# Performance work log

Measured on AMD Instinct MI355X. Metric: run time of the kernel, lower is better.

The kernel has to match this reference:

```python
import jax, jax.numpy as jnp
import numpy as np

B, C, DD, HH, WW = 1, 128, 16, 16, 16
D_STATE, D_CONV, EXPAND = 16, 4, 2
D_INNER = EXPAND * C
DT_RANK = (C + 15) // 16


def setup_inputs():
    key = jax.random.key(0)
    ks = jax.random.split(key, 10)
    def w(k, shape, s=0.02):
        return jax.random.normal(k, shape, dtype=jnp.float32) * s
    return {
        "x": jax.random.normal(ks[0], (B, C, DD, HH, WW), dtype=jnp.float32),
        "ln_w": jnp.ones((C,), jnp.float32),
        "ln_b": jnp.zeros((C,), jnp.float32),
        "mnorm_w": jnp.ones((C,), jnp.float32),
        "mnorm_b": jnp.zeros((C,), jnp.float32),
        "in_proj_w": w(ks[1], (2 * D_INNER, C)),
        "conv_w": w(ks[2], (D_INNER, D_CONV), 0.2),
        "conv_b": jnp.zeros((D_INNER,), jnp.float32),
        "x_proj_w": w(ks[3], (DT_RANK + 2 * D_STATE, D_INNER)),
        "dt_proj_w": w(ks[4], (D_INNER, DT_RANK), 0.1),
        "dt_proj_b": jnp.full((D_INNER,), float(np.log(np.expm1(0.01))), jnp.float32),
        "A_log": jnp.log(jnp.tile(jnp.arange(1, D_STATE + 1, dtype=jnp.float32), (D_INNER, 1))),
        "D_param": jnp.ones((D_INNER,), jnp.float32),
        "out_proj_w": w(ks[5], (C, D_INNER)),
        "proj_w": w(ks[6], (C, 3 * C)),
        "proj_b": jnp.zeros((C,), jnp.float32),
        "fc1_w": w(ks[7], (4 * C, C)),
        "fc1_b": jnp.zeros((4 * C,), jnp.float32),
        "fc2_w": w(ks[8], (C, 4 * C)),
        "fc2_b": jnp.zeros((C,), jnp.float32),
    }


def _ln_cf(x, w, b, eps=1e-6):
    # channels_first LayerNorm over axis 1 (matches custom LayerNorm)
    u = x.mean(1, keepdims=True)
    s = ((x - u) ** 2).mean(1, keepdims=True)
    xn = (x - u) * jax.lax.rsqrt(s + eps)
    return w[None, :, None, None, None] * xn + b[None, :, None, None, None]


def _ln_last(x, w, b, eps=1e-5):
    u = x.mean(-1, keepdims=True)
    s = ((x - u) ** 2).mean(-1, keepdims=True)
    return (x - u) * jax.lax.rsqrt(s + eps) * w + b


def _selective_scan(u, delta, A, Bm, Cm, Dv):
    # u, delta: (N,L,d); Bm,Cm: (N,L,n); A: (d,n); Dv: (d,)
    dA = jnp.exp(delta[..., None] * A)                               # (N,L,d,n)
    dBu = delta[..., None] * Bm[:, :, None, :] * u[..., None]         # (N,L,d,n)
    def step(h, inp):
        dA_t, dBu_t, C_t = inp
        h = dA_t * h + dBu_t
        y = jnp.einsum("bdn,bn->bd", h, C_t)
        return h, y
    h0 = jnp.zeros((u.shape[0], A.shape[0], A.shape[1]), u.dtype)
    _, ys = jax.lax.scan(step, h0, (dA.swapaxes(0, 1), dBu.swapaxes(0, 1), Cm.swapaxes(0, 1)))
    return ys.swapaxes(0, 1) + u * Dv


def _mamba(xin, in_proj_w, conv_w, conv_b, x_proj_w, dt_proj_w, dt_proj_b, A_log, D_param, out_proj_w):
    # xin: (N, L, C)
    N, L, _ = xin.shape
    xz = xin @ in_proj_w.T                                            # (N,L,2*d_inner)
    xr, z = jnp.split(xz, 2, axis=-1)
    # causal depthwise conv1d, kernel D_CONV, left-padded (mamba conv1d[..., :L])
    xp = jnp.pad(xr, ((0, 0), (D_CONV - 1, 0), (0, 0)))
    xc = sum(conv_w[:, k] * xp[:, k:k + L, :] for k in range(D_CONV)) + conv_b
    xc = jax.nn.silu(xc)
    x_dbl = xc @ x_proj_w.T                                           # (N,L,dt_rank+2n)
    dt = x_dbl[..., :DT_RANK]
    Bm = x_dbl[..., DT_RANK:DT_RANK + D_STATE]
    Cm = x_dbl[..., DT_RANK + D_STATE:]
    delta = jax.nn.softplus(dt @ dt_proj_w.T + dt_proj_b)
    A = -jnp.exp(A_log)
    y = _selective_scan(xc, delta, A, Bm, Cm, D_param)
    y = y * jax.nn.silu(z)
    return y @ out_proj_w.T


def _forward(x, ln_w, ln_b, mnorm_w, mnorm_b, in_proj_w, conv_w, conv_b, x_proj_w, dt_proj_w, dt_proj_b, A_log, D_param, out_proj_w, proj_w, proj_b, fc1_w, fc1_b, fc2_w, fc2_b):
    Bb, Cc, Dd, Hh, Ww = x.shape
    L = Dd * Hh * Ww
    x1 = _ln_cf(x, ln_w, ln_b)
    # three directional flattenings (d-, h-, w-major); cube => shapes identical
    xd = x1.reshape(Bb, Cc, L)
    xh = x1.transpose(0, 1, 3, 4, 2).reshape(Bb, Cc, L)
    xw = x1.transpose(0, 1, 4, 2, 3).reshape(Bb, Cc, L)
    seq = jnp.stack([xd, xh, xw], 0).reshape(3 * Bb, Cc, L).swapaxes(1, 2)  # (3B,L,C)
    seq = _ln_last(seq, mnorm_w, mnorm_b)
    y = _mamba(seq, in_proj_w, conv_w, conv_b, x_proj_w, dt_proj_w, dt_proj_b, A_log, D_param, out_proj_w)
    # reassemble per-direction volumes (no inverse permute, matching torch code) and concat on channels
    cat = y.swapaxes(1, 2).reshape(3, Bb, Cc, Dd, Hh, Ww).transpose(1, 0, 2, 3, 4, 5).reshape(Bb, 3 * Cc, Dd, Hh, Ww)
    out1 = jnp.einsum("bkdhw,ok->bodhw", cat, proj_w) + proj_b[None, :, None, None, None]
    out_res = x + out1
    h = _ln_cf(out_res, ln_w, ln_b)
    h = jnp.einsum("bcdhw,oc->bodhw", h, fc1_w) + fc1_b[None, :, None, None, None]
    h = jax.nn.gelu(h, approximate=False)
    h = jnp.einsum("bcdhw,oc->bodhw", h, fc2_w) + fc2_b[None, :, None, None, None]
    return h + out_res


def reference(x, ln_w, ln_b, mnorm_w, mnorm_b, in_proj_w, conv_w, conv_b, x_proj_w, dt_proj_w, dt_proj_b, A_log, D_param, out_proj_w, proj_w, proj_b, fc1_w, fc1_b, fc2_w, fc2_b):
    return _forward(x, ln_w, ln_b, mnorm_w, mnorm_b, in_proj_w, conv_w, conv_b, x_proj_w, dt_proj_w, dt_proj_b, A_log, D_param, out_proj_w, proj_w, proj_b, fc1_w, fc1_b, fc2_w, fc2_b)
```

## Files before the change

### kernel.cpp

```cpp
#include <hip/hip_runtime.h>
#include <hip/hip_bf16.h>
#include <math.h>

#define L 4096
#define C 128
#define DI 256
#define NST 16
#define NS 3
#define NCH 256
#define CT 16
#define R3 12288

__device__ __forceinline__ float siluf(float x){ return x / (1.f + __expf(-x)); }
__device__ __forceinline__ float geluf(float x){ return 0.5f*x*(1.f + erff(x*0.70710678118654752f)); }

__device__ __forceinline__ int permf(int s, int l){
  if(s==0) return l;
  if(s==1) return ((l&15)<<8) | ((l>>8)<<4) | ((l>>4)&15);
  return (((l>>4)&15)<<8) | ((l&15)<<4) | (l>>8);
}

__global__ void k_M(const float* __restrict__ opw, const float* __restrict__ pw,
                    float* __restrict__ Mw){
  int b = blockIdx.x;
  int o = b & 127, s = b >> 7;
  int d = threadIdx.x;
  float acc = 0.f;
  for(int c=0;c<C;c++) acc += opw[c*DI + d] * pw[o*384 + s*128 + c];
  Mw[(s*256+d)*128 + o] = acc;
}

__global__ void k_lngemm(const float* __restrict__ x, const float* __restrict__ lw,
                         const float* __restrict__ lb, const float* __restrict__ mw,
                         const float* __restrict__ mb, const float* __restrict__ ipw,
                         float* __restrict__ Z){
  __shared__ float As[128][68];
  __shared__ float Bs[64][132];
  int p0 = blockIdx.x*64, j0 = blockIdx.y*64;
  int tid = threadIdx.x;
  for(int q=0;q<8;q++){
    int f = q*1024 + tid*4; int cc = f>>6, p = f&63;
    float4 v = *(const float4*)&x[cc*L + p0 + p];
    *(float4*)&As[cc][p] = v;
  }
  for(int q=0;q<8;q++){
    int f = q*1024 + tid*4; int j = f>>7, k = f&127;
    float4 b = *(const float4*)&ipw[(j0+j)*C + k];
    *(float4*)&Bs[j][k] = b;
  }
  __syncthreads();
  {
    int p = tid>>2, kg = tid&3;
    float s=0.f, sq=0.f;
    #pragma unroll
    for(int i=0;i<32;i++){
      int k = kg*32 + ((i + kg*2)&31);
      float v = As[k][p]; s += v; sq += v*v;
    }
    s  += __shfl_xor(s,1);  s  += __shfl_xor(s,2);
    sq += __shfl_xor(sq,1); sq += __shfl_xor(sq,2);
    float m1 = s*(1.f/C);
    float r1 = rsqrtf(sq*(1.f/C) - m1*m1 + 1e-6f);
    float s2=0.f, sq2=0.f;
    #pragma unroll
    for(int i=0;i<32;i++){
      int k = kg*32 + ((i + kg*2)&31);
      float t = lw[k]*((As[k][p]-m1)*r1) + lb[k];
      s2 += t; sq2 += t*t;
    }
    s2  += __shfl_xor(s2,1);  s2  += __shfl_xor(s2,2);
    sq2 += __shfl_xor(sq2,1); sq2 += __shfl_xor(sq2,2);
    float m2 = s2*(1.f/C);
    float r2 = rsqrtf(sq2*(1.f/C) - m2*m2 + 1e-5f);
    #pragma unroll
    for(int i=0;i<32;i++){
      int k = kg*32 + ((i + kg*2)&31);
      float t = lw[k]*((As[k][p]-m1)*r1) + lb[k];
      As[k][p] = mw[k]*((t-m2)*r2) + mb[k];
    }
  }
  __syncthreads();
  int og = tid & 15, r4 = tid >> 4;
  float acc[4][4] = {};
  for(int k=0;k<128;k++){
    float4 av = *(const float4*)&As[k][r4*4];
    float a[4] = {av.x, av.y, av.z, av.w};
    float b[4];
    #pragma unroll
    for(int j=0;j<4;j++) b[j] = Bs[og+16*j][k];
    #pragma unroll
    for(int i=0;i<4;i++)
      #pragma unroll
      for(int j=0;j<4;j++) acc[i][j] += a[i]*b[j];
  }
  #pragma unroll
  for(int i=0;i<4;i++)
    #pragma unroll
    for(int j=0;j<4;j++)
      Z[(p0+r4*4+i)*512 + j0 + og + 16*j] = acc[i][j];
}

__global__ void k_conv(const float* __restrict__ Z, const float* __restrict__ cw,
                       const float* __restrict__ cb, float* __restrict__ xc){
  int bl = blockIdx.x;
  int s = bl >> 12, l = bl & 4095;
  int d = threadIdx.x;
  float acc = cb[d];
  #pragma unroll
  for(int k=0;k<4;k++){
    int lk = l - 3 + k;
    if(lk >= 0){
      int p = permf(s, lk);
      acc += cw[d*4+k] * Z[p*512 + d];
    }
  }
  xc[bl*DI + d] = siluf(acc);
}

__global__ void k_xd3(const float* __restrict__ xc, const float* __restrict__ xpw,
                      const float* __restrict__ dtw, const float* __restrict__ dtb,
                      float* __restrict__ Bc, float* __restrict__ Cc,
                      float* __restrict__ delta){
  __shared__ float Ast[256][65];
  __shared__ float BCs[40][65];
  int r0 = blockIdx.x*64;
  int tid = threadIdx.x;
  for(int q=0;q<16;q++){
    int f = q*1024 + tid*4; int row = f>>8, k = f&255;
    float4 v = *(const float4*)&xc[(r0+row)*DI + k];
    Ast[k+0][row]=v.x; Ast[k+1][row]=v.y; Ast[k+2][row]=v.z; Ast[k+3][row]=v.w;
  }
  __syncthreads();
  int lane = tid & 63;
  int cb0 = __builtin_amdgcn_readfirstlane((tid>>6)*10);
  const float* wp = xpw + cb0*DI;
  float acc[10] = {0.f,0.f,0.f,0.f,0.f,0.f,0.f,0.f,0.f,0.f};
  for(int k4=0;k4<64;k4++){
    int k = k4*4;
    float a0 = Ast[k+0][lane], a1 = Ast[k+1][lane];
    float a2 = Ast[k+2][lane], a3 = Ast[k+3][lane];
    #pragma unroll
    for(int j=0;j<10;j++){
      float4 w = *(const float4*)&wp[j*DI + k];
      acc[j] += a0*w.x + a1*w.y + a2*w.z + a3*w.w;
    }
  }
  #pragma unroll
  for(int j=0;j<10;j++) BCs[cb0+j][lane] = acc[j];
  __syncthreads();
  {
    float4 ww0 = *(const float4*)&dtw[tid*8];
    float4 ww1 = *(const float4*)&dtw[tid*8+4];
    float bb = dtb[tid];
    for(int r=0;r<64;r++){
      float aa = bb + BCs[0][r]*ww0.x + BCs[1][r]*ww0.y + BCs[2][r]*ww0.z + BCs[3][r]*ww0.w
                    + BCs[4][r]*ww1.x + BCs[5][r]*ww1.y + BCs[6][r]*ww1.z + BCs[7][r]*ww1.w;
      delta[(r0+r)*DI + tid] = (aa > 20.f) ? aa : log1pf(__expf(aa));
    }
  }
  {
    int r = tid>>2, ng = (tid&3)*4;
    float4 bv = make_float4(BCs[ 8+ng][r], BCs[ 9+ng][r], BCs[10+ng][r], BCs[11+ng][r]);
    float4 cv = make_float4(BCs[24+ng][r], BCs[25+ng][r], BCs[26+ng][r], BCs[27+ng][r]);
    *(float4*)&Bc[(r0+r)*NST + ng] = bv;
    *(float4*)&Cc[(r0+r)*NST + ng] = cv;
  }
}

__global__ void k_scanA(const float* __restrict__ delta, const float* __restrict__ xc,
                        const float* __restrict__ Bc, const float* __restrict__ A_log,
                        float* __restrict__ aggA, float* __restrict__ aggB){
  int b = blockIdx.x;
  int ng = b & 3, ch = (b>>2)&255, s = b>>10;
  int d = threadIdx.x;
  int n0 = ng*4;
  float Aa[4], P[4] = {1.f,1.f,1.f,1.f}, S[4] = {0.f,0.f,0.f,0.f};
  #pragma unroll
  for(int j=0;j<4;j++) Aa[j] = -__expf(A_log[d*NST + n0 + j]);
  int base = s*L + ch*CT;
  #pragma unroll
  for(int st=0; st<CT; st++){
    int row = base + st;
    float dl = delta[row*DI + d];
    float u  = xc[row*DI + d];
    float4 bv = *(const float4*)&Bc[row*NST + n0];
    float dlu = dl*u;
    float a;
    a = __expf(dl*Aa[0]); S[0] = a*S[0] + dlu*bv.x; P[0] *= a;
    a = __expf(dl*Aa[1]); S[1] = a*S[1] + dlu*bv.y; P[1] *= a;
    a = __expf(dl*Aa[2]); S[2] = a*S[2] + dlu*bv.z; P[2] *= a;
    a = __expf(dl*Aa[3]); S[3] = a*S[3] + dlu*bv.w; P[3] *= a;
  }
  int idx0 = ch*R3 + s*256 + d;
  #pragma unroll
  for(int j=0;j<4;j++){
    int idx = idx0 + (n0+j)*768;
    aggA[idx] = P[j]; aggB[idx] = S[j];
  }
}

__global__ void k_scanB(const float* __restrict__ aggA, const float* __restrict__ aggB,
                        float* __restrict__ hIn){
  __shared__ float PA[32][9], PB[32][9];
  int tid = threadIdx.x;
  int jl = tid & 31, seg = tid >> 5;
  int j = blockIdx.x*32 + jl;
  int c0 = seg*32;
  float pa[32], pb[32];
  float P = 1.f, S = 0.f;
  #pragma unroll
  for(int i=0;i<32;i++){
    pa[i] = P; pb[i] = S;
    float a = aggA[(c0+i)*R3 + j], b = aggB[(c0+i)*R3 + j];
    S = a*S + b; P = a*P;
  }
  PA[jl][seg] = P; PB[jl][seg] = S;
  __syncthreads();
  if(tid < 32){
    float h = 0.f;
    #pragma unroll
    for(int sg=0; sg<8; sg++){
      float p = PA[tid][sg], s2 = PB[tid][sg];
      PA[tid][sg] = h;
      h = p*h + s2;
    }
  }
  __syncthreads();
  float h0 = PA[jl][seg];
  #pragma unroll
  for(int i=0;i<32;i++){
    hIn[(c0+i)*R3 + j] = pa[i]*h0 + pb[i];
  }
}

__global__ void k_scanC(const float* __restrict__ delta, const float* __restrict__ xc,
                        const float* __restrict__ Bc, const float* __restrict__ Cc,
                        const float* __restrict__ A_log, const float* __restrict__ Dp,
                        const float* __restrict__ Z, const float* __restrict__ hIn,
                        float* __restrict__ yz){
  int b = blockIdx.x;
  int ch = b & 255, s = b >> 8;
  int d = threadIdx.x;
  float Aa[16], h[16];
  #pragma unroll
  for(int n=0;n<16;n++) Aa[n] = -__expf(A_log[d*NST + n]);
  #pragma unroll
  for(int n=0;n<16;n++) h[n] = hIn[ch*R3 + n*768 + s*256 + d];
  float Dv = Dp[d];
  int base = s*L + ch*CT;
  #pragma unroll 2
  for(int st=0; st<CT; st++){
    int row = base + st;
    float dl = delta[row*DI + d];
    float u  = xc[row*DI + d];
    float dlu = dl*u;
    const float4* Bp = (const float4*)&Bc[row*NST];
    const float4* Cp = (const float4*)&Cc[row*NST];
    float y = u*Dv;
    #pragma unroll
    for(int q=0;q<4;q++){
      float4 bv = Bp[q], cv = Cp[q];
      float a;
      a = __expf(dl*Aa[4*q+0]); h[4*q+0] = a*h[4*q+0] + dlu*bv.x; y += h[4*q+0]*cv.x;
      a = __expf(dl*Aa[4*q+1]); h[4*q+1] = a*h[4*q+1] + dlu*bv.y; y += h[4*q+1]*cv.y;
      a = __expf(dl*Aa[4*q+2]); h[4*q+2] = a*h[4*q+2] + dlu*bv.z; y += h[4*q+2]*cv.z;
      a = __expf(dl*Aa[4*q+3]); h[4*q+3] = a*h[4*q+3] + dlu*bv.w; y += h[4*q+3]*cv.w;
    }
    int l = ch*CT + st;
    int p = permf(s, l);
    float zv = Z[p*512 + 256 + d];
    yz[(s*L + l)*DI + d] = y * siluf(zv);
  }
}

__global__ void k_proj(const float* __restrict__ yz, const float* __restrict__ Mw,
                       float* __restrict__ pp){
  __shared__ float As[64][68];
  __shared__ float Bs[64][132];
  int p0 = blockIdx.x*64; int kc = blockIdx.y;
  int s = kc >> 1, d0 = (kc & 1)*128;
  int tid = threadIdx.x;
  int og = tid & 15, r4 = tid >> 4;
  float acc[4][8] = {};
  for(int kk=0; kk<2; kk++){
    int kb = d0 + kk*64;
    for(int q=0;q<4;q++){
      int f = q*1024 + tid*4; int r = f>>6, k = f&63;
      float4 a = *(const float4*)&yz[(s*L + p0 + r)*DI + kb + k];
      *(float4*)&As[r][k] = a;
    }
    for(int q=0;q<8;q++){
      int f = q*1024 + tid*4; int k = f>>7, o = f&127;
      float4 b = *(const float4*)&Mw[(s*256 + kb + k)*128 + o];
      *(float4*)&Bs[k][o] = b;
    }
    __syncthreads();
    for(int k=0;k<64;k++){
      float a[4];
      #pragma unroll
      for(int i=0;i<4;i++) a[i] = As[r4*4+i][k];
      #pragma unroll
      for(int j=0;j<8;j++){
        float bb = Bs[k][og+16*j];
        #pragma unroll
        for(int i=0;i<4;i++) acc[i][j] += a[i]*bb;
      }
    }
    __syncthreads();
  }
  float* dst = pp + kc*524288;
  #pragma unroll
  for(int i=0;i<4;i++)
    #pragma unroll
    for(int j=0;j<8;j++)
      dst[(p0+r4*4+i)*C + og + 16*j] = acc[i][j];
}

__global__ void k_pred(const float* __restrict__ pp, const float* __restrict__ x,
                       const float* __restrict__ pb, float* __restrict__ ores){
  __shared__ float Xs[16][129];
  int p0 = blockIdx.x*16; int tid = threadIdx.x;
  for(int q=0;q<8;q++){
    int f = q*256 + tid; int pl = f&15, o = f>>4;
    Xs[pl][o] = x[o*L + p0 + pl];
  }
  __syncthreads();
  for(int q=0;q<8;q++){
    int f = q*256 + tid; int o = f&127, pl = f>>7;
    int idx = (p0+pl)*C + o;
    float v = pp[idx] + pp[524288+idx] + pp[1048576+idx]
            + pp[1572864+idx] + pp[2097152+idx] + pp[2621440+idx];
    ores[idx] = v + Xs[pl][o] + pb[o];
  }
}

__global__ void k_fc1(const float* __restrict__ ores, const float* __restrict__ lw,
                      const float* __restrict__ lb, const float* __restrict__ w1,
                      const float* __restrict__ b1, float* __restrict__ H){
  __shared__ float As[64][129];
  __shared__ float Bs[64][129];
  int p0 = blockIdx.x*64, j0 = blockIdx.y*64;
  int tid = threadIdx.x;
  for(int q=0;q<8;q++){
    int f = q*1024 + tid*4; int r = f>>7, k = f&127;
    float4 a = *(const float4*)&ores[(p0+r)*C + k];
    As[r][k]=a.x; As[r][k+1]=a.y; As[r][k+2]=a.z; As[r][k+3]=a.w;
    float4 b = *(const float4*)&w1[(j0+r)*C + k];
    Bs[r][k]=b.x; Bs[r][k+1]=b.y; Bs[r][k+2]=b.z; Bs[r][k+3]=b.w;
  }
  __syncthreads();
  {
    int r = tid>>2, kg = tid&3;
    float s=0.f, sq=0.f;
    #pragma unroll
    for(int i=0;i<32;i++){
      int k = kg*32 + ((i + kg*8)&31);
      float v = As[r][k]; s += v; sq += v*v;
    }
    s  += __shfl_xor(s,1);  s  += __shfl_xor(s,2);
    sq += __shfl_xor(sq,1); sq += __shfl_xor(sq,2);
    float m1 = s*(1.f/C);
    float r1 = rsqrtf(sq*(1.f/C) - m1*m1 + 1e-6f);
    #pragma unroll
    for(int i=0;i<32;i++){
      int k = kg*32 + ((i + kg*8)&31);
      As[r][k] = lw[k]*((As[r][k]-m1)*r1) + lb[k];
    }
  }
  __syncthreads();
  int og = tid & 15, r4 = tid >> 4;
  float acc[4][4] = {};
  for(int k=0;k<128;k++){
    float a[4], b[4];
    #pragma unroll
    for(int i=0;i<4;i++) a[i] = As[r4*4+i][k];
    #pragma unroll
    for(int j=0;j<4;j++) b[j] = Bs[og+16*j][k];
    #pragma unroll
    for(int i=0;i<4;i++)
      #pragma unroll
      for(int j=0;j<4;j++) acc[i][j] += a[i]*b[j];
  }
  #pragma unroll
  for(int i=0;i<4;i++)
    #pragma unroll
    for(int j=0;j<4;j++){
      int jj = j0 + og + 16*j;
      H[(p0+r4*4+i)*512 + jj] = geluf(acc[i][j] + b1[jj]);
    }
}

__global__ void k_fc2(const float* __restrict__ H, const float* __restrict__ w2,
                      float* __restrict__ fp){
  __shared__ float As[64][68];
  __shared__ float Bs[128][68];
  int p0 = blockIdx.x*64; int kc = blockIdx.y;
  int tid = threadIdx.x;
  int og = tid & 15, r4 = tid >> 4;
  float acc[4][8] = {};
  for(int kk=0; kk<2; kk++){
    int kb = kc*128 + kk*64;
    for(int q=0;q<4;q++){
      int f = q*1024 + tid*4; int r = f>>6, k = f&63;
      float4 a = *(const float4*)&H[(p0+r)*512 + kb + k];
      *(float4*)&As[r][k] = a;
    }
    for(int q=0;q<8;q++){
      int f = q*1024 + tid*4; int o = f>>6, k = f&63;
      float4 b = *(const float4*)&w2[o*512 + kb + k];
      *(float4*)&Bs[o][k] = b;
    }
    __syncthreads();
    for(int k=0;k<64;k++){
      float a[4];
      #pragma unroll
      for(int i=0;i<4;i++) a[i] = As[r4*4+i][k];
      #pragma unroll
      for(int j=0;j<8;j++){
        float bb = Bs[og+16*j][k];
        #pragma unroll
        for(int i=0;i<4;i++) acc[i][j] += a[i]*bb;
      }
    }
    __syncthreads();
  }
  float* dst = fp + kc*524288;
  #pragma unroll
  for(int i=0;i<4;i++)
    #pragma unroll
    for(int j=0;j<8;j++)
      dst[(p0+r4*4+i)*C + og + 16*j] = acc[i][j];
}

__global__ void k_fred(const float* __restrict__ fp, const float* __restrict__ b2,
                       const float* __restrict__ ores, float* __restrict__ out){
  __shared__ float S[128][17];
  int p0 = blockIdx.x*16; int tid = threadIdx.x;
  for(int q=0;q<8;q++){
    int f = q*256 + tid; int o = f&127, pl = f>>7;
    int idx = (p0+pl)*C + o;
    float v = fp[idx] + fp[524288+idx] + fp[1048576+idx] + fp[1572864+idx];
    S[o][pl] = v + b2[o] + ores[idx];
  }
  __syncthreads();
  for(int q=0;q<8;q++){
    int f = q*256 + tid; int pl = f&15, o = f>>4;
    out[o*L + p0 + pl] = S[o][pl];
  }
}

extern "C" void kernel_launch(void* const* d_in, const int* in_sizes, int n_in,
                              void* d_out, int out_size, void* d_ws, size_t ws_size,
                              hipStream_t stream) {
  const float* x     = (const float*)d_in[0];
  const float* ln_w  = (const float*)d_in[1];
  const float* ln_b  = (const float*)d_in[2];
  const float* mw    = (const float*)d_in[3];
  const float* mb    = (const float*)d_in[4];
  const float* ipw   = (const float*)d_in[5];
  const float* cw    = (const float*)d_in[6];
  const float* cb    = (const float*)d_in[7];
  const float* xpw   = (const float*)d_in[8];
  const float* dtw   = (const float*)d_in[9];
  const float* dtb   = (const float*)d_in[10];
  const float* A_log = (const float*)d_in[11];
  const float* Dp    = (const float*)d_in[12];
  const float* opw   = (const float*)d_in[13];
  const float* pw    = (const float*)d_in[14];
  const float* pb    = (const float*)d_in[15];
  const float* w1    = (const float*)d_in[16];
  const float* b1    = (const float*)d_in[17];
  const float* w2    = (const float*)d_in[18];
  const float* b2    = (const float*)d_in[19];
  float* out = (float*)d_out;

  float* ws = (float*)d_ws;
  float* Z     = ws;
  float* xc    = Z     + 2097152;
  float* delta = xc    + 3145728;
  float* dt    = delta + 3145728;
  float* Bc    = dt    + 98304;
  float* Cc    = Bc    + 196608;
  float* aggA  = Cc    + 196608;
  float* aggB  = aggA  + 3145728;
  float* hIn   = aggB  + 3145728;
  float* Mw    = hIn   + 3145728;
  float* ores  = Mw    + 98304;
  (void)dt;
  float* yz = aggA;
  float* pp = delta;
  float* H  = Z;
  float* fp = xc;

  k_M     <<<384, 256, 0, stream>>>(opw, pw, Mw);
  k_lngemm<<<dim3(64,8), 256, 0, stream>>>(x, ln_w, ln_b, mw, mb, ipw, Z);
  k_conv  <<<NS*L, 256, 0, stream>>>(Z, cw, cb, xc);
  k_xd3   <<<192, 256, 0, stream>>>(xc, xpw, dtw, dtb, Bc, Cc, delta);
  k_scanA <<<3072, 256, 0, stream>>>(delta, xc, Bc, A_log, aggA, aggB);
  k_scanB <<<384, 256, 0, stream>>>(aggA, aggB, hIn);
  k_scanC <<<768, 256, 0, stream>>>(delta, xc, Bc, Cc, A_log, Dp, Z, hIn, yz);
  k_proj  <<<dim3(64,6), 256, 0, stream>>>(yz, Mw, pp);
  k_pred  <<<256, 256, 0, stream>>>(pp, x, pb, ores);
  k_fc1   <<<dim3(64,8), 256, 0, stream>>>(ores, ln_w, ln_b, w1, b1, H);
  k_fc2   <<<dim3(64,4), 256, 0, stream>>>(H, w2, fp);
  k_fred  <<<256, 256, 0, stream>>>(fp, b2, ores, out);
}
```

Measured before the change: 292.6 us.

## Split x_proj GEMM into split-K tiled kernel plus separate dt/B/C epilogue

Replaces the single 192-block x_proj+dt_proj kernel with two kernels. The first computes partial x_proj products with split-K over two halves, using 768 blocks with shared-memory tiles of activations and weights. The second sums the partials and applies dt_proj, softplus and the B/C scatter over 768 blocks. This raises parallelism on a kernel that under-filled the GPU, at the cost of an extra launch and an intermediate buffer round-trip through global memory.

Result: faster. 274.3 us (-6.3%).

```diff
diff --git a/kernel.cpp b/kernel.cpp
--- a/kernel.cpp
+++ b/kernel.cpp
@@ -117,53 +117,71 @@
   xc[bl*DI + d] = siluf(acc);
 }
 
-__global__ void k_xd3(const float* __restrict__ xc, const float* __restrict__ xpw,
-                      const float* __restrict__ dtw, const float* __restrict__ dtb,
-                      float* __restrict__ Bc, float* __restrict__ Cc,
-                      float* __restrict__ delta){
-  __shared__ float Ast[256][65];
-  __shared__ float BCs[40][65];
-  int r0 = blockIdx.x*64;
-  int tid = threadIdx.x;
-  for(int q=0;q<16;q++){
-    int f = q*1024 + tid*4; int row = f>>8, k = f&255;
-    float4 v = *(const float4*)&xc[(r0+row)*DI + k];
-    Ast[k+0][row]=v.x; Ast[k+1][row]=v.y; Ast[k+2][row]=v.z; Ast[k+3][row]=v.w;
-  }
-  __syncthreads();
-  int lane = tid & 63;
-  int cb0 = __builtin_amdgcn_readfirstlane((tid>>6)*10);
-  const float* wp = xpw + cb0*DI;
-  float acc[10] = {0.f,0.f,0.f,0.f,0.f,0.f,0.f,0.f,0.f,0.f};
-  for(int k4=0;k4<64;k4++){
-    int k = k4*4;
-    float a0 = Ast[k+0][lane], a1 = Ast[k+1][lane];
-    float a2 = Ast[k+2][lane], a3 = Ast[k+3][lane];
-    #pragma unroll
-    for(int j=0;j<10;j++){
-      float4 w = *(const float4*)&wp[j*DI + k];
-      acc[j] += a0*w.x + a1*w.y + a2*w.z + a3*w.w;
-    }
-  }
-  #pragma unroll
-  for(int j=0;j<10;j++) BCs[cb0+j][lane] = acc[j];
+__global__ void k_xd4a(const float* __restrict__ xc, const float* __restrict__ xpw,
+                       float* __restrict__ xp){
+  __shared__ float As[32][132];
+  __shared__ float Ws[40][132];
+  int r0 = blockIdx.x*32;
+  int k0 = blockIdx.y*128;
+  int tid = threadIdx.x;
+  for(int q=0;q<4;q++){
+    int f = q*256 + tid; int r = f>>5, kk = (f&31)*4;
+    float4 v = *(const float4*)&xc[(r0+r)*DI + k0 + kk];
+    *(float4*)&As[r][kk] = v;
+  }
+  for(int q=0;q<5;q++){
+    int f = q*256 + tid; int col = f>>5, kk = (f&31)*4;
+    float4 v = *(const float4*)&xpw[col*DI + k0 + kk];
+    *(float4*)&Ws[col][kk] = v;
+  }
+  __syncthreads();
+  int r = tid & 31, cg = tid >> 5;
+  float acc[5] = {0.f,0.f,0.f,0.f,0.f};
+  for(int k4=0;k4<32;k4++){
+    float4 a = *(const float4*)&As[r][k4*4];
+    #pragma unroll
+    for(int j=0;j<5;j++){
+      float4 w = *(const float4*)&Ws[cg*5+j][k4*4];
+      acc[j] += a.x*w.x + a.y*w.y + a.z*w.z + a.w*w.w;
+    }
+  }
+  float* dst = xp + (blockIdx.y*12288 + r0 + r)*40 + cg*5;
+  #pragma unroll
+  for(int j=0;j<5;j++) dst[j] = acc[j];
+}
+
+__global__ void k_xd4b(const float* __restrict__ xp, const float* __restrict__ dtw,
+                       const float* __restrict__ dtb, float* __restrict__ Bc,
+                       float* __restrict__ Cc, float* __restrict__ delta){
+  __shared__ float xdb[40][17];
+  int r0 = blockIdx.x*16;
+  int tid = threadIdx.x;
+  for(int e=tid; e<640; e+=256){
+    int row = e/40, col = e%40;
+    int idx = (r0+row)*40 + col;
+    xdb[col][row] = xp[idx] + xp[491520 + idx];
+  }
   __syncthreads();
   {
     float4 ww0 = *(const float4*)&dtw[tid*8];
     float4 ww1 = *(const float4*)&dtw[tid*8+4];
     float bb = dtb[tid];
-    for(int r=0;r<64;r++){
-      float aa = bb + BCs[0][r]*ww0.x + BCs[1][r]*ww0.y + BCs[2][r]*ww0.z + BCs[3][r]*ww0.w
-                    + BCs[4][r]*ww1.x + BCs[5][r]*ww1.y + BCs[6][r]*ww1.z + BCs[7][r]*ww1.w;
+    #pragma unroll 4
+    for(int r=0;r<16;r++){
+      float aa = bb + xdb[0][r]*ww0.x + xdb[1][r]*ww0.y + xdb[2][r]*ww0.z + xdb[3][r]*ww0.w
+                    + xdb[4][r]*ww1.x + xdb[5][r]*ww1.y + xdb[6][r]*ww1.z + xdb[7][r]*ww1.w;
       delta[(r0+r)*DI + tid] = (aa > 20.f) ? aa : log1pf(__expf(aa));
     }
   }
-  {
-    int r = tid>>2, ng = (tid&3)*4;
-    float4 bv = make_float4(BCs[ 8+ng][r], BCs[ 9+ng][r], BCs[10+ng][r], BCs[11+ng][r]);
-    float4 cv = make_float4(BCs[24+ng][r], BCs[25+ng][r], BCs[26+ng][r], BCs[27+ng][r]);
-    *(float4*)&Bc[(r0+r)*NST + ng] = bv;
-    *(float4*)&Cc[(r0+r)*NST + ng] = cv;
+  if(tid < 64){
+    int rr = tid>>2, ng = (tid&3)*4;
+    float4 bv = make_float4(xdb[8+ng][rr], xdb[9+ng][rr], xdb[10+ng][rr], xdb[11+ng][rr]);
+    *(float4*)&Bc[(r0+rr)*NST + ng] = bv;
+  } else if(tid < 128){
+    int t2 = tid - 64;
+    int rr = t2>>2, ng = (t2&3)*4;
+    float4 cv = make_float4(xdb[24+ng][rr], xdb[25+ng][rr], xdb[26+ng][rr], xdb[27+ng][rr]);
+    *(float4*)&Cc[(r0+rr)*NST + ng] = cv;
   }
 }
 
@@ -487,6 +505,7 @@
   float* Mw    = hIn   + 3145728;
   float* ores  = Mw    + 98304;
   (void)dt;
+  float* xp = hIn;
   float* yz = aggA;
   float* pp = delta;
   float* H  = Z;
@@ -495,7 +514,8 @@
   k_M     <<<384, 256, 0, stream>>>(opw, pw, Mw);
   k_lngemm<<<dim3(64,8), 256, 0, stream>>>(x, ln_w, ln_b, mw, mb, ipw, Z);
   k_conv  <<<NS*L, 256, 0, stream>>>(Z, cw, cb, xc);
-  k_xd3   <<<192, 256, 0, stream>>>(xc, xpw, dtw, dtb, Bc, Cc, delta);
+  k_xd4a  <<<dim3(384,2), 256, 0, stream>>>(xc, xpw, xp);
+  k_xd4b  <<<768, 256, 0, stream>>>(xp, dtw, dtb, Bc, Cc, delta);
   k_scanA <<<3072, 256, 0, stream>>>(delta, xc, Bc, A_log, aggA, aggB);
   k_scanB <<<384, 256, 0, stream>>>(aggA, aggB, hIn);
   k_scanC <<<768, 256, 0, stream>>>(delta, xc, Bc, Cc, A_log, Dp, Z, hIn, yz);
```
